# Kernel optimization log

Hardware: AMD Instinct MI355X
Metric: run time of the kernel (lower is better)

## Reference

```python
import jax, jax.numpy as jnp
import numpy as np
import itertools as it
from math import factorial

DIM, N = 3, 30
K = 2 * DIM * N + 1          # 181
P = factorial(N) // factorial(N - DIM)  # 24360
DEMB = DIM * DIM + K         # 190

# permutation index tables (trace-time constants)
_combs = np.array(list(it.permutations(range(N), DIM)), dtype=np.int32)          # (P, DIM)
_rest = np.array([sorted(set(range(N)) - set(map(int, c))) for c in _combs],
                 dtype=np.int32)                                                  # (P, N-DIM)


def setup_inputs() -> dict:
    key = jax.random.key(0)
    k0, k1, k2, k3, k4 = jax.random.split(key, 5)
    return {
        "matrix": jax.random.normal(k0, (DIM, N), dtype=jnp.float32),
        "Ws_in": jax.random.normal(k1, (K, DIM), dtype=jnp.float32),        # inner weights_sort
        "Wd_in": jax.random.normal(k2, (K, N - DIM), dtype=jnp.float32),    # inner weights_dot
        "Ws_out": jax.random.normal(k3, (K, DEMB), dtype=jnp.float32),      # outer weights_sort
        "Wd_out": jax.random.normal(k4, (K, P), dtype=jnp.float32),         # outer weights_dot
    }


def reference(matrix, Ws_in, Wd_in, Ws_out, Wd_out):
    combs = jnp.asarray(_combs)   # (P, DIM)
    rest = jnp.asarray(_rest)     # (P, N-DIM)
    cols = matrix.T               # (N, DIM) -- columns of the cloud as rows

    # UpperGram, batched over all P permutations
    Xd = cols[combs].transpose(0, 2, 1)   # (P, DIM, DIM) selected columns
    Xr = cols[rest].transpose(0, 2, 1)    # (P, DIM, N-DIM) remaining columns (sorted)
    gram = jnp.einsum('pdi,pdj->pij', Xd, Xd)          # Xd^T Xd, (P, DIM, DIM)
    # torch flattens gram.transpose(1,0); gram is exactly symmetric so this equals row-major
    gram_flat = gram.transpose(0, 2, 1).reshape(P, DIM * DIM)
    proj = jnp.einsum('pdi,pdm->pim', Xd, Xr)          # Xd^T Xrest, (P, DIM, N-DIM)

    # inner Embed (non-original branch), batched over P
    sm = jnp.einsum('pim,ki->pmk', proj, Ws_in)        # (P, N-DIM, K)
    sm_sorted = jnp.sort(sm, axis=1)                   # column-wise sort (dim=0 in torch)
    emb = jnp.einsum('km,pmk->pk', Wd_in, sm_sorted)   # diag(Wd @ sorted), (P, K)

    vec = jnp.concatenate([gram_flat, emb], axis=1)    # (P, DEMB); torch's vec before .t()

    # outer Embed (original branch) on mat = vec.T (DEMB, P)
    sm2 = vec @ Ws_out.T                               # mat^T @ Ws^T, (P, K)
    sm2_sorted = jnp.sort(sm2, axis=0)                 # sort over permutation axis
    out = jnp.einsum('kp,pk->k', Wd_out, sm2_sorted)   # diag(Wd @ sorted), (K,)
    return out
```

## Files before the change

kernel.cpp:

```cpp
#include <hip/hip_runtime.h>
#include <hip/hip_bf16.h>

#define DIMK 3
#define NPTS 30
#define KK   181
#define PP   24360
#define DEMB 190
#define VLD  192
#define SNP  24576

typedef __attribute__((ext_vector_type(8))) short bf16x8;
typedef __attribute__((ext_vector_type(4))) float f32x4;
typedef __attribute__((ext_vector_type(2))) __fp16 h2;

__device__ __forceinline__ ushort f2bf(float f) {
    unsigned u = __float_as_uint(f);
    u += 0x7FFFu + ((u >> 16) & 1u);
    return (ushort)(u >> 16);
}

__global__ __launch_bounds__(1024, 2) void k_inner(
    const float* __restrict__ M,
    const float* __restrict__ Ws_in,
    const float* __restrict__ Wd_in,
    const float* __restrict__ Wout,
    ushort* __restrict__ Abf,
    ushort* __restrict__ vec)
{
    __shared__ float Gs[NPTS * 32];
    __shared__ float WsS[192 * 3];
    __shared__ float WdS[192 * 28];

    const int tid = threadIdx.x;

    {
        int gid = blockIdx.x * 1024 + tid;
        if (gid < 192 * 192) {
            int k = gid / 192, d = gid - k * 192;
            Abf[gid] = (k < KK && d < DEMB) ? f2bf(Wout[k * DEMB + d]) : (ushort)0;
        }
    }

    for (int i = tid; i < 192 * 3; i += 1024) WsS[i] = (i < KK * 3) ? Ws_in[i] : 0.f;
    for (int i = tid; i < 192 * 28; i += 1024) {
        int k = i / 28, m = i - k * 28;
        WdS[i] = (k < KK && m < 27) ? Wd_in[k * 27 + m] : 0.f;
    }
    for (int e = tid; e < NPTS * 32; e += 1024) {
        int a = e >> 5, b = e & 31;
        Gs[e] = (b < NPTS)
            ? (M[a] * M[b] + M[NPTS + a] * M[NPTS + b] + M[2 * NPTS + a] * M[2 * NPTS + b])
            : 0.f;
    }
    __syncthreads();

    const int wave = tid >> 6;
    const int lane = tid & 63;
    const int wid = blockIdx.x * 16 + wave;
    const int chunk = wid % 3;
    const int pstream = wid / 3;
    const int nstream = (chunk == 2) ? 2730 : 2731;
    const int k = chunk * 64 + lane;

    const float INF = __builtin_inff();
    const bool kvalid = (k < KK);
    const float w0 = WsS[k * 3 + 0];
    const float w1 = WsS[k * 3 + 1];
    const float w2 = WsS[k * 3 + 2];
    const float* wd = WdS + k * 28;

    const int NPAIR = PP / 2;

    for (int t = pstream; t < NPAIR; t += nstream) {
        const int p0 = 2 * t;
        int i0 = p0 / 812;
        int r  = p0 - i0 * 812;
        int i1 = r / 28;
        int i2 = r - i1 * 28;
        int c0 = i0;
        int c1 = i1 + (i1 >= c0 ? 1 : 0);
        int lo = min(c0, c1), hi = max(c0, c1);
        int c2a = i2;
        if (c2a >= lo) c2a++;
        if (c2a >= hi) c2a++;
        int c2b = i2 + 1;
        if (c2b >= lo) c2b++;
        if (c2b >= hi) c2b++;

        ushort* vrow0 = vec + (long)p0 * VLD;
        ushort* vrow1 = vrow0 + VLD;

        if (chunk == 0 && lane < 9) {
            int i = lane / 3, j = lane % 3;
            int cia = (i == 0) ? c0 : ((i == 1) ? c1 : c2a);
            int cja = (j == 0) ? c0 : ((j == 1) ? c1 : c2a);
            vrow0[lane] = f2bf(Gs[(cia << 5) + cja]);
            int cib = (i == 0) ? c0 : ((i == 1) ? c1 : c2b);
            int cjb = (j == 0) ? c0 : ((j == 1) ? c1 : c2b);
            vrow1[lane] = f2bf(Gs[(cib << 5) + cjb]);
        }

        const float* g0 = Gs + (c0 << 5);
        const float* g1 = Gs + (c1 << 5);
        const float* ga = Gs + (c2a << 5);
        const float* gb = Gs + (c2b << 5);
        const unsigned basem = (1u << c0) | (1u << c1);
        const unsigned maska = basem | (1u << c2a);
        const unsigned maskb = basem | (1u << c2b);

        h2 s[30];
#pragma unroll
        for (int q = 0; q < 8; ++q) {
            float4 x0 = *(const float4*)&g0[q * 4];
            float4 x1 = *(const float4*)&g1[q * 4];
            float4 xa = *(const float4*)&ga[q * 4];
            float4 xb = *(const float4*)&gb[q * 4];
            int j0 = q * 4;
            if (j0 + 0 < NPTS) {
                float c = w0 * x0.x + w1 * x1.x;
                float va = w2 * xa.x + c;
                float vb = w2 * xb.x + c;
                va = ((maska >> (j0 + 0)) & 1u) ? INF : va;
                vb = ((maskb >> (j0 + 0)) & 1u) ? INF : vb;
                s[j0 + 0] = __builtin_amdgcn_cvt_pkrtz(va, vb);
            }
            if (j0 + 1 < NPTS) {
                float c = w0 * x0.y + w1 * x1.y;
                float va = w2 * xa.y + c;
                float vb = w2 * xb.y + c;
                va = ((maska >> (j0 + 1)) & 1u) ? INF : va;
                vb = ((maskb >> (j0 + 1)) & 1u) ? INF : vb;
                s[j0 + 1] = __builtin_amdgcn_cvt_pkrtz(va, vb);
            }
            if (j0 + 2 < NPTS) {
                float c = w0 * x0.z + w1 * x1.z;
                float va = w2 * xa.z + c;
                float vb = w2 * xb.z + c;
                va = ((maska >> (j0 + 2)) & 1u) ? INF : va;
                vb = ((maskb >> (j0 + 2)) & 1u) ? INF : vb;
                s[j0 + 2] = __builtin_amdgcn_cvt_pkrtz(va, vb);
            }
            if (j0 + 3 < NPTS) {
                float c = w0 * x0.w + w1 * x1.w;
                float va = w2 * xa.w + c;
                float vb = w2 * xb.w + c;
                va = ((maska >> (j0 + 3)) & 1u) ? INF : va;
                vb = ((maskb >> (j0 + 3)) & 1u) ? INF : vb;
                s[j0 + 3] = __builtin_amdgcn_cvt_pkrtz(va, vb);
            }
        }

#pragma unroll
        for (int pw = 1; pw < 32; pw <<= 1) {
#pragma unroll
            for (int kk = pw; kk >= 1; kk >>= 1) {
#pragma unroll
                for (int j = kk % pw; j + kk < 32; j += 2 * kk) {
#pragma unroll
                    for (int i = 0; i < kk; ++i) {
                        int a = i + j, b = i + j + kk;
                        if (a / (pw * 2) == b / (pw * 2) && b < 30
                            && !(pw == 16 && a == 27)) {
                            h2 x = s[a], y = s[b];
                            s[a] = __builtin_elementwise_min(x, y);
                            s[b] = __builtin_elementwise_max(x, y);
                        }
                    }
                }
            }
        }

        if (kvalid) {
            float emb0 = 0.f, emb1 = 0.f;
#pragma unroll
            for (int j = 0; j < 24; j += 4) {
                float4 w4 = *(const float4*)&wd[j];
                emb0 += w4.x * (float)s[j + 0].x + w4.y * (float)s[j + 1].x
                      + w4.z * (float)s[j + 2].x + w4.w * (float)s[j + 3].x;
                emb1 += w4.x * (float)s[j + 0].y + w4.y * (float)s[j + 1].y
                      + w4.z * (float)s[j + 2].y + w4.w * (float)s[j + 3].y;
            }
            {
                float4 w4 = *(const float4*)&wd[24];
                emb0 += w4.x * (float)s[24].x + w4.y * (float)s[25].x
                      + w4.z * (float)s[26].x;
                emb1 += w4.x * (float)s[24].y + w4.y * (float)s[25].y
                      + w4.z * (float)s[26].y;
            }
            vrow0[9 + k] = f2bf(emb0);
            vrow1[9 + k] = f2bf(emb1);
        } else if (k < 183) {
            vrow0[9 + k] = 0;
            vrow1[9 + k] = 0;
        }
    }
}

__global__ __launch_bounds__(256) void k_gemm(
    const ushort* __restrict__ vecB,
    const ushort* __restrict__ Abf,
    ushort* __restrict__ sm2TP)
{
    const int tid  = threadIdx.x;
    const int bid  = blockIdx.x;
    const int tile = bid >> 2;
    const int qtr  = bid & 3;
    const int wave = tid >> 6;
    const int lane = tid & 63;
    const int n = lane & 15;
    const int quad = lane >> 4;
    const int p = tile * 64 + wave * 16 + n;

    bf16x8 bfrag[6];
    if (p < PP) {
        const ushort* row = vecB + (long)p * VLD;
#pragma unroll
        for (int kc = 0; kc < 6; ++kc)
            bfrag[kc] = *(const bf16x8*)&row[kc * 32 + quad * 8];
    } else {
        bf16x8 z = {0, 0, 0, 0, 0, 0, 0, 0};
#pragma unroll
        for (int kc = 0; kc < 6; ++kc) bfrag[kc] = z;
    }

#pragma unroll
    for (int i = 0; i < 3; ++i) {
        const int kt = qtr * 3 + i;
        f32x4 acc = {0.f, 0.f, 0.f, 0.f};
        const ushort* arow = Abf + (kt * 16 + n) * 192;
#pragma unroll
        for (int kc = 0; kc < 6; ++kc) {
            bf16x8 afrag = *(const bf16x8*)&arow[kc * 32 + quad * 8];
            acc = __builtin_amdgcn_mfma_f32_16x16x32_bf16(afrag, bfrag[kc], acc, 0, 0, 0);
        }
        int k0 = kt * 16 + quad * 4;
#pragma unroll
        for (int r = 0; r < 4; ++r) {
            int kg = k0 + r;
            if (kg < KK) {
                unsigned e;
                if (p < PP) {
                    unsigned u = __float_as_uint(acc[r]);
                    u = (u & 0x80000000u) ? ~u : (u | 0x80000000u);
                    e = (u + 0x8000u) >> 16;
                } else {
                    e = 0xFFFFu;
                }
                sm2TP[(long)kg * SNP + p] = (ushort)e;
            }
        }
    }
}

#define WAVES  16
#define WCHUNK 1536

__device__ __forceinline__ unsigned long long matchany8(unsigned d) {
    unsigned long long m = ~0ull;
#pragma unroll
    for (int b = 0; b < 8; ++b) {
        unsigned bit = (d >> b) & 1u;
        unsigned long long bal = __ballot(bit);
        m &= bit ? bal : ~bal;
    }
    return m;
}

__device__ __forceinline__ void scan_hist(unsigned* cntC, unsigned* cntZ,
                                          unsigned* tot, int tid) {
    if (tid < 256) {
        unsigned run = 0;
        for (int w = 0; w < WAVES; ++w) {
            unsigned t = cntC[w * 256 + tid];
            cntC[w * 256 + tid] = run;
            run += t;
        }
        tot[tid] = run;
    }
    __syncthreads();
    if (tid < 64) {
        unsigned t0 = tot[tid * 4], t1 = tot[tid * 4 + 1];
        unsigned t2 = tot[tid * 4 + 2], t3 = tot[tid * 4 + 3];
        unsigned s = t0 + t1 + t2 + t3;
        unsigned sc = s;
#pragma unroll
        for (int off = 1; off < 64; off <<= 1) {
            unsigned o = (unsigned)__shfl_up((int)sc, off, 64);
            if (tid >= off) sc += o;
        }
        unsigned ex = sc - s;
        tot[tid * 4]     = ex + t0;
        tot[tid * 4 + 1] = ex + t0 + t1;
        tot[tid * 4 + 2] = ex + t0 + t1 + t2;
        tot[tid * 4 + 3] = ex + s;
    } else if (cntZ) {
        for (int i = tid - 64; i < WAVES * 256; i += 1024 - 64) cntZ[i] = 0;
    }
    __syncthreads();
    for (int i = tid; i < WAVES * 256; i += 1024) {
        int d = i & 255;
        unsigned db = (d == 0) ? 0u : tot[d - 1];
        cntC[i] += db;
    }
    __syncthreads();
}

__global__ __launch_bounds__(1024) void k_sort(
    const ushort* __restrict__ sm2TP,
    const float* __restrict__ WdOut,
    float* __restrict__ out)
{
    __shared__ ushort keysL[SNP];
    __shared__ unsigned cntA[WAVES * 256];
    __shared__ unsigned cntB[WAVES * 256];
    __shared__ unsigned tot[256];
    __shared__ float red[WAVES];

    const int tid  = threadIdx.x;
    const int wave = tid >> 6;
    const int lane = tid & 63;
    const int k    = blockIdx.x;

    const ushort* rowU = sm2TP + (long)k * SNP;
    const float* wrow  = WdOut + (long)k * PP;

    const int base_idx = wave * WCHUNK + lane;
    const int wbase = wave * 256;
    const unsigned long long lt_mask = (1ull << lane) - 1ull;

    for (int i = tid; i < WAVES * 256; i += 1024) cntA[i] = 0;
    __syncthreads();

    for (int j = 0; j < 24; ++j) {
        unsigned u = rowU[base_idx + j * 64];
        atomicAdd(&cntA[wbase + (u & 255u)], 1u);
    }
    __syncthreads();
    scan_hist(cntA, cntB, tot, tid);

    for (int j = 0; j < 24; ++j) {
        unsigned u = rowU[base_idx + j * 64];
        unsigned d = u & 255u;
        unsigned long long mm = matchany8(d);
        int leader = __ffsll(mm) - 1;
        unsigned myrank = (unsigned)__popcll(mm & lt_mask);
        unsigned old = 0;
        if (lane == leader)
            old = atomicAdd(&cntA[wbase + d], (unsigned)__popcll(mm));
        old = (unsigned)__shfl((int)old, leader, 64);
        unsigned dest = old + myrank;
        keysL[dest] = (ushort)u;
        atomicAdd(&cntB[(dest / WCHUNK) * 256 + (u >> 8)], 1u);
    }
    __syncthreads();
    scan_hist(cntB, (unsigned*)0, tot, tid);

    float local = 0.f;
    for (int j = 0; j < 24; ++j) {
        unsigned u = keysL[base_idx + j * 64];
        unsigned d = u >> 8;
        unsigned long long mm = matchany8(d);
        int leader = __ffsll(mm) - 1;
        unsigned myrank = (unsigned)__popcll(mm & lt_mask);
        unsigned old = 0;
        if (lane == leader)
            old = atomicAdd(&cntB[wbase + d], (unsigned)__popcll(mm));
        old = (unsigned)__shfl((int)old, leader, 64);
        unsigned dest = old + myrank;
        if (dest < PP) {
            unsigned raw16 = (u & 0x8000u) ? (u & 0x7FFFu) : ((~u) & 0xFFFFu);
            local += wrow[dest] * __uint_as_float(raw16 << 16);
        }
    }

#pragma unroll
    for (int off = 32; off > 0; off >>= 1)
        local += __shfl_down(local, off, 64);
    if (lane == 0) red[wave] = local;
    __syncthreads();
    if (tid < WAVES) {
        float x = red[tid];
#pragma unroll
        for (int off = 8; off > 0; off >>= 1)
            x += __shfl_down(x, off, 64);
        if (tid == 0) out[k] = x;
    }
}

extern "C" void kernel_launch(void* const* d_in, const int* in_sizes, int n_in,
                              void* d_out, int out_size, void* d_ws, size_t ws_size,
                              hipStream_t stream) {
    const float* M      = (const float*)d_in[0];
    const float* Ws_in  = (const float*)d_in[1];
    const float* Wd_in  = (const float*)d_in[2];
    const float* Ws_out = (const float*)d_in[3];
    const float* Wd_out = (const float*)d_in[4];
    float* out = (float*)d_out;

    char* ws = (char*)d_ws;
    ushort* vecB  = (ushort*)ws;
    ushort* sm2TP = (ushort*)(ws + (size_t)PP * VLD * 2);
    ushort* Abf   = (ushort*)(ws + (size_t)PP * VLD * 2 + (size_t)KK * SNP * 2);

    k_inner<<<512, 1024, 0, stream>>>(M, Ws_in, Wd_in, Ws_out, Abf, vecB);

    k_gemm<<<(SNP / 64) * 4, 256, 0, stream>>>(vecB, Abf, sm2TP);

    k_sort<<<KK, 1024, 0, stream>>>(sm2TP, Wd_out, out);
}
```

Before: 196.6 us.

## Replace per-row radix sort with 16-bit key histogram counting sort split across blocks

The two-pass LSD radix sort per output row is replaced by a direct counting approach. Four blocks per row each build a 16384-bin shared histogram over a quarter of the 16-bit key space, count the keys below their range, prefix-scan the bins, and accumulate weight times value for each rank range; partial sums are combined with atomicAdd into the zeroed output. The GEMM kernel also swaps operand roles so each lane writes four contiguous 16-bit keys in one vector store, and it stages the vec tile through LDS. This trades the matchany ballot loops and scatter passes for larger histograms and more blocks, at the cost of float atomics and serial per-bin loops when many keys share a bin.

```diff
diff --git a/kernel.cpp b/kernel.cpp
--- a/kernel.cpp
+++ b/kernel.cpp
@@ -12,6 +12,7 @@
 typedef __attribute__((ext_vector_type(8))) short bf16x8;
 typedef __attribute__((ext_vector_type(4))) float f32x4;
 typedef __attribute__((ext_vector_type(2))) __fp16 h2;
+typedef __attribute__((ext_vector_type(4))) ushort u16x4;
 
 __device__ __forceinline__ ushort f2bf(float f) {
     unsigned u = __float_as_uint(f);
@@ -199,8 +200,11 @@
 __global__ __launch_bounds__(256) void k_gemm(
     const ushort* __restrict__ vecB,
     const ushort* __restrict__ Abf,
-    ushort* __restrict__ sm2TP)
+    ushort* __restrict__ sm2TP,
+    float* __restrict__ out)
 {
+    __shared__ ushort vs[64 * 200];
+
     const int tid  = threadIdx.x;
     const int bid  = blockIdx.x;
     const int tile = bid >> 2;
@@ -209,35 +213,48 @@
     const int lane = tid & 63;
     const int n = lane & 15;
     const int quad = lane >> 4;
-    const int p = tile * 64 + wave * 16 + n;
-
-    bf16x8 bfrag[6];
-    if (p < PP) {
-        const ushort* row = vecB + (long)p * VLD;
+
+    if (bid == 0 && tid < KK) out[tid] = 0.f;
+
+    {
+        const char* src = (const char*)(vecB + (size_t)tile * 64 * VLD);
+#pragma unroll
+        for (int it = 0; it < 6; ++it) {
+            int byte = (it * 256 + tid) * 16;
+            int row = byte / 384;
+            int col = byte - row * 384;
+            bf16x8 d = *(const bf16x8*)(src + byte);
+            *(bf16x8*)((char*)vs + row * 400 + col) = d;
+        }
+    }
+    __syncthreads();
+
+    bf16x8 afrag[6];
+    {
+        const char* base = (const char*)vs + (wave * 16 + n) * 400;
 #pragma unroll
         for (int kc = 0; kc < 6; ++kc)
-            bfrag[kc] = *(const bf16x8*)&row[kc * 32 + quad * 8];
-    } else {
-        bf16x8 z = {0, 0, 0, 0, 0, 0, 0, 0};
-#pragma unroll
-        for (int kc = 0; kc < 6; ++kc) bfrag[kc] = z;
-    }
+            afrag[kc] = *(const bf16x8*)(base + kc * 64 + quad * 16);
+    }
+
+    const int pb = tile * 64 + wave * 16 + quad * 4;
 
 #pragma unroll
     for (int i = 0; i < 3; ++i) {
         const int kt = qtr * 3 + i;
+        const int kg = kt * 16 + n;
         f32x4 acc = {0.f, 0.f, 0.f, 0.f};
-        const ushort* arow = Abf + (kt * 16 + n) * 192;
+        const ushort* arow = Abf + kg * 192;
 #pragma unroll
         for (int kc = 0; kc < 6; ++kc) {
-            bf16x8 afrag = *(const bf16x8*)&arow[kc * 32 + quad * 8];
-            acc = __builtin_amdgcn_mfma_f32_16x16x32_bf16(afrag, bfrag[kc], acc, 0, 0, 0);
-        }
-        int k0 = kt * 16 + quad * 4;
-#pragma unroll
-        for (int r = 0; r < 4; ++r) {
-            int kg = k0 + r;
-            if (kg < KK) {
+            bf16x8 bfrag = *(const bf16x8*)&arow[kc * 32 + quad * 8];
+            acc = __builtin_amdgcn_mfma_f32_16x16x32_bf16(afrag[kc], bfrag, acc, 0, 0, 0);
+        }
+        if (kg < KK) {
+            u16x4 st;
+#pragma unroll
+            for (int r = 0; r < 4; ++r) {
+                int p = pb + r;
                 unsigned e;
                 if (p < PP) {
                     unsigned u = __float_as_uint(acc[r]);
@@ -246,144 +263,103 @@
                 } else {
                     e = 0xFFFFu;
                 }
-                sm2TP[(long)kg * SNP + p] = (ushort)e;
-            }
-        }
-    }
-}
-
-#define WAVES  16
-#define WCHUNK 1536
-
-__device__ __forceinline__ unsigned long long matchany8(unsigned d) {
-    unsigned long long m = ~0ull;
-#pragma unroll
-    for (int b = 0; b < 8; ++b) {
-        unsigned bit = (d >> b) & 1u;
-        unsigned long long bal = __ballot(bit);
-        m &= bit ? bal : ~bal;
-    }
-    return m;
-}
-
-__device__ __forceinline__ void scan_hist(unsigned* cntC, unsigned* cntZ,
-                                          unsigned* tot, int tid) {
-    if (tid < 256) {
-        unsigned run = 0;
-        for (int w = 0; w < WAVES; ++w) {
-            unsigned t = cntC[w * 256 + tid];
-            cntC[w * 256 + tid] = run;
-            run += t;
-        }
-        tot[tid] = run;
-    }
-    __syncthreads();
-    if (tid < 64) {
-        unsigned t0 = tot[tid * 4], t1 = tot[tid * 4 + 1];
-        unsigned t2 = tot[tid * 4 + 2], t3 = tot[tid * 4 + 3];
-        unsigned s = t0 + t1 + t2 + t3;
-        unsigned sc = s;
-#pragma unroll
-        for (int off = 1; off < 64; off <<= 1) {
-            unsigned o = (unsigned)__shfl_up((int)sc, off, 64);
-            if (tid >= off) sc += o;
-        }
-        unsigned ex = sc - s;
-        tot[tid * 4]     = ex + t0;
-        tot[tid * 4 + 1] = ex + t0 + t1;
-        tot[tid * 4 + 2] = ex + t0 + t1 + t2;
-        tot[tid * 4 + 3] = ex + s;
-    } else if (cntZ) {
-        for (int i = tid - 64; i < WAVES * 256; i += 1024 - 64) cntZ[i] = 0;
-    }
-    __syncthreads();
-    for (int i = tid; i < WAVES * 256; i += 1024) {
-        int d = i & 255;
-        unsigned db = (d == 0) ? 0u : tot[d - 1];
-        cntC[i] += db;
-    }
-    __syncthreads();
-}
-
-__global__ __launch_bounds__(1024) void k_sort(
+                st[r] = (ushort)e;
+            }
+            *(u16x4*)&sm2TP[(size_t)kg * SNP + pb] = st;
+        }
+    }
+}
+
+#define HB 16384
+
+__global__ __launch_bounds__(1024, 2) void k_hist(
     const ushort* __restrict__ sm2TP,
     const float* __restrict__ WdOut,
     float* __restrict__ out)
 {
-    __shared__ ushort keysL[SNP];
-    __shared__ unsigned cntA[WAVES * 256];
-    __shared__ unsigned cntB[WAVES * 256];
-    __shared__ unsigned tot[256];
-    __shared__ float red[WAVES];
+    __shared__ unsigned hist[HB];
+    __shared__ unsigned wred[16];
+    __shared__ unsigned wscan[16];
+    __shared__ float fred[16];
 
     const int tid  = threadIdx.x;
     const int wave = tid >> 6;
     const int lane = tid & 63;
-    const int k    = blockIdx.x;
-
-    const ushort* rowU = sm2TP + (long)k * SNP;
-    const float* wrow  = WdOut + (long)k * PP;
-
-    const int base_idx = wave * WCHUNK + lane;
-    const int wbase = wave * 256;
-    const unsigned long long lt_mask = (1ull << lane) - 1ull;
-
-    for (int i = tid; i < WAVES * 256; i += 1024) cntA[i] = 0;
-    __syncthreads();
-
+    const int k = blockIdx.x >> 2;
+    const int q = blockIdx.x & 3;
+    const unsigned base = (unsigned)q * HB;
+
+    const ushort* rowU = sm2TP + (size_t)k * SNP;
+    const float* wrow  = WdOut + (size_t)k * PP;
+
+    for (int i = tid; i < HB; i += 1024) hist[i] = 0u;
+    __syncthreads();
+
+    unsigned below = 0;
     for (int j = 0; j < 24; ++j) {
-        unsigned u = rowU[base_idx + j * 64];
-        atomicAdd(&cntA[wbase + (u & 255u)], 1u);
-    }
-    __syncthreads();
-    scan_hist(cntA, cntB, tot, tid);
-
-    for (int j = 0; j < 24; ++j) {
-        unsigned u = rowU[base_idx + j * 64];
-        unsigned d = u & 255u;
-        unsigned long long mm = matchany8(d);
-        int leader = __ffsll(mm) - 1;
-        unsigned myrank = (unsigned)__popcll(mm & lt_mask);
-        unsigned old = 0;
-        if (lane == leader)
-            old = atomicAdd(&cntA[wbase + d], (unsigned)__popcll(mm));
-        old = (unsigned)__shfl((int)old, leader, 64);
-        unsigned dest = old + myrank;
-        keysL[dest] = (ushort)u;
-        atomicAdd(&cntB[(dest / WCHUNK) * 256 + (u >> 8)], 1u);
-    }
-    __syncthreads();
-    scan_hist(cntB, (unsigned*)0, tot, tid);
-
-    float local = 0.f;
-    for (int j = 0; j < 24; ++j) {
-        unsigned u = keysL[base_idx + j * 64];
-        unsigned d = u >> 8;
-        unsigned long long mm = matchany8(d);
-        int leader = __ffsll(mm) - 1;
-        unsigned myrank = (unsigned)__popcll(mm & lt_mask);
-        unsigned old = 0;
-        if (lane == leader)
-            old = atomicAdd(&cntB[wbase + d], (unsigned)__popcll(mm));
-        old = (unsigned)__shfl((int)old, leader, 64);
-        unsigned dest = old + myrank;
-        if (dest < PP) {
-            unsigned raw16 = (u & 0x8000u) ? (u & 0x7FFFu) : ((~u) & 0xFFFFu);
-            local += wrow[dest] * __uint_as_float(raw16 << 16);
+        unsigned u = rowU[tid + j * 1024];
+        below += (u < base) ? 1u : 0u;
+        unsigned rel = u - base;
+        if (rel < (unsigned)HB) atomicAdd(&hist[rel], 1u);
+    }
+    {
+        unsigned b = below;
+#pragma unroll
+        for (int off = 32; off > 0; off >>= 1)
+            b += (unsigned)__shfl_down((int)b, off, 64);
+        if (lane == 0) wred[wave] = b;
+    }
+    __syncthreads();
+    unsigned below_tot = 0;
+#pragma unroll
+    for (int w = 0; w < 16; ++w) below_tot += wred[w];
+
+    unsigned loc[16];
+    unsigned tsum = 0;
+#pragma unroll
+    for (int bq = 0; bq < 16; ++bq) {
+        loc[bq] = tsum;
+        tsum += hist[tid * 16 + bq];
+    }
+    unsigned inc = tsum;
+#pragma unroll
+    for (int off = 1; off < 64; off <<= 1) {
+        unsigned o = (unsigned)__shfl_up((int)inc, off, 64);
+        if (lane >= off) inc += o;
+    }
+    if (lane == 63) wscan[wave] = inc;
+    __syncthreads();
+    unsigned wbase = 0;
+#pragma unroll
+    for (int w = 0; w < 16; ++w) wbase += (w < wave) ? wscan[w] : 0u;
+
+    unsigned r0 = below_tot + wbase + (inc - tsum);
+
+    float acc = 0.f;
+#pragma unroll
+    for (int bq = 0; bq < 16; ++bq) {
+        unsigned c = hist[tid * 16 + bq];
+        if (c) {
+            unsigned key = base + (unsigned)tid * 16 + bq;
+            unsigned raw16 = (key & 0x8000u) ? (key & 0x7FFFu) : ((~key) & 0xFFFFu);
+            float val = __uint_as_float(raw16 << 16);
+            unsigned r = r0 + loc[bq];
+            unsigned cl = (r < (unsigned)PP) ? min(c, (unsigned)PP - r) : 0u;
+            for (unsigned j = 0; j < cl; ++j)
+                acc += wrow[r + j] * val;
         }
     }
 
 #pragma unroll
     for (int off = 32; off > 0; off >>= 1)
-        local += __shfl_down(local, off, 64);
-    if (lane == 0) red[wave] = local;
-    __syncthreads();
-    if (tid < WAVES) {
-        float x = red[tid];
-#pragma unroll
-        for (int off = 8; off > 0; off >>= 1)
-            x += __shfl_down(x, off, 64);
-        if (tid == 0) out[k] = x;
+        acc += __shfl_down(acc, off, 64);
+    if (lane == 0) fred[wave] = acc;
+    __syncthreads();
+    if (tid == 0) {
+        float t = 0.f;
+#pragma unroll
+        for (int w = 0; w < 16; ++w) t += fred[w];
+        atomicAdd(&out[k], t);
     }
 }
 
@@ -404,7 +380,7 @@
 
     k_inner<<<512, 1024, 0, stream>>>(M, Ws_in, Wd_in, Ws_out, Abf, vecB);
 
-    k_gemm<<<(SNP / 64) * 4, 256, 0, stream>>>(vecB, Abf, sm2TP);
-
-    k_sort<<<KK, 1024, 0, stream>>>(sm2TP, Wd_out, out);
-}
+    k_gemm<<<(SNP / 64) * 4, 256, 0, stream>>>(vecB, Abf, sm2TP, out);
+
+    k_hist<<<KK * 4, 1024, 0, stream>>>(sm2TP, Wd_out, out);
+}
```

Result: slower. 676.6 us (+244.1%).
